# Kernel optimization log

Measured on AMD Instinct MI355X. Metric: run time of the kernel, lower is better.

Reference implementation:

```python
import jax, jax.numpy as jnp
import numpy as np

NUM_HEADS = 16
NEG = -1e9

def setup_inputs() -> dict:
    key = jax.random.key(0)
    ks = jax.random.split(key, 5)
    B, S, D = 4, 2048, 1024
    scale = 1.0 / np.sqrt(D)
    return {
        "x": jax.random.normal(ks[0], (B, S, D), dtype=jnp.float32),
        "WQ": jax.random.normal(ks[1], (D, D), dtype=jnp.float32) * scale,
        "WK": jax.random.normal(ks[2], (D, D), dtype=jnp.float32) * scale,
        "WV": jax.random.normal(ks[3], (D, D), dtype=jnp.float32) * scale,
        "WO": jax.random.normal(ks[4], (D, D), dtype=jnp.float32) * scale,
    }

def _split_heads(t, h):
    # [..., s, h*d] -> [..., h, s, d]
    *lead, s, hd = t.shape
    return jnp.swapaxes(t.reshape(*lead, s, h, hd // h), -3, -2)

def reference(x, WQ, WK, WV, WO):
    h = NUM_HEADS
    S = x.shape[-2]
    # Linear stores weight [out, in]; y = x @ W^T
    Q = _split_heads(x @ WQ.T, h)  # [b,h,s,dk]
    K = _split_heads(x @ WK.T, h)
    V = _split_heads(x @ WV.T, h)
    dk = Q.shape[-1]
    scores = jnp.einsum('bhqd,bhkd->bhqk', Q, K) / jnp.sqrt(jnp.float32(dk))
    causal = jnp.tril(jnp.ones((S, S), dtype=bool))  # allowed positions
    scores = jnp.where(causal, scores, NEG)
    # explicit stable softmax (matches source)
    m = jnp.max(scores, axis=-1, keepdims=True)
    e = jnp.exp(scores - m)
    attn = e / jnp.sum(e, axis=-1, keepdims=True)
    out = jnp.einsum('bhqk,bhkd->bhqd', attn, V)  # [b,h,s,dv]
    out = jnp.swapaxes(out, -3, -2).reshape(*x.shape[:-1], -1)  # [b,s,h*dv]
    return out @ WO.T
```

## Files before the change

### kernel.cpp

```cpp
#include <hip/hip_runtime.h>
#include <stdint.h>
#include <math.h>

typedef __attribute__((ext_vector_type(8))) short bf16x8;
typedef __attribute__((ext_vector_type(4))) short v4s;
typedef __attribute__((ext_vector_type(4))) float f32x4;
typedef __attribute__((ext_vector_type(4))) unsigned short u16x4;
typedef __attribute__((ext_vector_type(2))) unsigned int u32x2;

#define MFMA16(a,b,c)   __builtin_amdgcn_mfma_f32_16x16x32_bf16((a),(b),(c),0,0,0)
#define MFMA16K(a,b,c)  __builtin_amdgcn_mfma_f32_16x16x16bf16_1k((a),(b),(c),0,0,0)

static __device__ __forceinline__ void gld_lds16(const void* g, void* l) {
  __builtin_amdgcn_global_load_lds(
      (const __attribute__((address_space(1))) unsigned int*)g,
      (__attribute__((address_space(3))) unsigned int*)l,
      16, 0, 0);
}

static __device__ __forceinline__ unsigned short f2bf(float f) {
  unsigned int u = __builtin_bit_cast(unsigned int, f);
  return (unsigned short)((u + 0x8000u) >> 16);
}

__global__ __launch_bounds__(256) void cvt_kernel(const float* __restrict__ in,
                                                  unsigned short* __restrict__ out,
                                                  int n4) {
  int i = blockIdx.x * blockDim.x + threadIdx.x;
  int stride = gridDim.x * blockDim.x;
  for (; i < n4; i += stride) {
    float4 v = ((const float4*)in)[i];
    u16x4 o;
    o.x = f2bf(v.x); o.y = f2bf(v.y); o.z = f2bf(v.z); o.w = f2bf(v.w);
    ((u16x4*)out)[i] = o;
  }
}

__global__ __launch_bounds__(256) void cvt4_kernel(const float* __restrict__ w0,
                                                   const float* __restrict__ w1,
                                                   const float* __restrict__ w2,
                                                   const float* __restrict__ w3,
                                                   unsigned short* __restrict__ out) {
  const float* in = (blockIdx.y == 0) ? w0 : (blockIdx.y == 1) ? w1
                  : (blockIdx.y == 2) ? w2 : w3;
  unsigned short* o = out + (size_t)blockIdx.y * 1048576;
  int i = blockIdx.x * blockDim.x + threadIdx.x;
  int stride = gridDim.x * blockDim.x;
  for (; i < 1048576/4; i += stride) {
    float4 v = ((const float4*)in)[i];
    u16x4 t;
    t.x = f2bf(v.x); t.y = f2bf(v.y); t.z = f2bf(v.z); t.w = f2bf(v.w);
    ((u16x4*)o)[i] = t;
  }
}

template<int MODE, typename CT>
__device__ __forceinline__ void gemm_bt_tile(const unsigned short* __restrict__ A,
                                             const unsigned short* __restrict__ Bt,
                                             CT* __restrict__ C,
                                             int m0, int n0)
{
  __shared__ __align__(16) unsigned short As[128*32];
  __shared__ __align__(16) unsigned short Bs[128*32];
  const int tid  = threadIdx.x;
  const int w    = tid >> 6, lane = tid & 63;
  const int quad = lane >> 4, c0 = lane & 15;
  const int wm   = w >> 1, wn = w & 1;

  const unsigned short* ga[2];
  const unsigned short* gb[2];
  int ldsoff[2];
  #pragma unroll
  for (int i = 0; i < 2; ++i) {
    int f = i*4096 + w*1024 + lane*16;
    int r = f >> 6;
    int q = (f >> 4) & 3;
    ga[i] = A  + (m0 + r)*1024 + q*8;
    gb[i] = Bt + (n0 + r)*1024 + q*8;
    ldsoff[i] = i*4096 + w*1024;
  }

  int aAddr[4], bAddr[4];
  #pragma unroll
  for (int t = 0; t < 4; ++t) {
    aAddr[t] = (wm*64 + t*16 + c0)*64 + quad*16;
    bAddr[t] = (wn*64 + t*16 + c0)*64 + quad*16;
  }

  f32x4 acc[4][4];
  #pragma unroll
  for (int i = 0; i < 4; ++i)
    #pragma unroll
    for (int j = 0; j < 4; ++j)
      acc[i][j] = (f32x4){0.f, 0.f, 0.f, 0.f};

  for (int kt = 0; kt < 32; ++kt) {
    __syncthreads();
    #pragma unroll
    for (int i = 0; i < 2; ++i) {
      gld_lds16(ga[i] + kt*32, (char*)As + ldsoff[i]);
      gld_lds16(gb[i] + kt*32, (char*)Bs + ldsoff[i]);
    }
    __syncthreads();

    bf16x8 af[4], bfr[4];
    #pragma unroll
    for (int t = 0; t < 4; ++t) af[t]  = *(const bf16x8*)((const char*)As + aAddr[t]);
    #pragma unroll
    for (int t = 0; t < 4; ++t) bfr[t] = *(const bf16x8*)((const char*)Bs + bAddr[t]);

    #pragma unroll
    for (int mt = 0; mt < 4; ++mt)
      #pragma unroll
      for (int nt = 0; nt < 4; ++nt)
        acc[mt][nt] = MFMA16(af[mt], bfr[nt], acc[mt][nt]);
  }

  const float scl = (MODE == 3) ? 0.1803368801f : 1.0f;
  #pragma unroll
  for (int mt = 0; mt < 4; ++mt) {
    #pragma unroll
    for (int nt = 0; nt < 4; ++nt) {
      if (MODE == 2) {
        u16x4 pk;
        #pragma unroll
        for (int r = 0; r < 4; ++r) pk[r] = f2bf(acc[mt][nt][r]);
        int s0 = m0 + wm*64 + mt*16 + quad*4;
        int gc = n0 + wn*64 + nt*16 + c0;
        int b = s0 >> 11, ss = s0 & 2047;
        int h = gc >> 6, d = gc & 63;
        *(u16x4*)((unsigned short*)C + (size_t)(((b << 4) + h)*64 + d)*2048 + ss) = pk;
      } else {
        #pragma unroll
        for (int r = 0; r < 4; ++r) {
          int gr = m0 + wm*64 + mt*16 + quad*4 + r;
          int gc = n0 + wn*64 + nt*16 + c0;
          if (MODE == 0 || MODE == 3) {
            int b = gr >> 11, s = gr & 2047;
            int h = gc >> 6, d = gc & 63;
            ((unsigned short*)C)[(((b << 4) + h)*2048 + s)*64 + d] = f2bf(acc[mt][nt][r] * scl);
          } else {
            ((float*)C)[gr*1024 + gc] = acc[mt][nt][r];
          }
        }
      }
    }
  }
}

__global__ __launch_bounds__(256) void qkv_kernel(
    const unsigned short* __restrict__ X,
    const unsigned short* __restrict__ WQ, const unsigned short* __restrict__ WK,
    const unsigned short* __restrict__ WV,
    unsigned short* __restrict__ Q, unsigned short* __restrict__ K,
    unsigned short* __restrict__ V)
{
  if (blockIdx.z == 2) {
    gemm_bt_tile<2>(X, WV, V, blockIdx.x*128, blockIdx.y*128);
  } else if (blockIdx.z == 0) {
    gemm_bt_tile<3>(X, WQ, Q, blockIdx.x*128, blockIdx.y*128);
  } else {
    gemm_bt_tile<0>(X, WK, K, blockIdx.x*128, blockIdx.y*128);
  }
}

__global__ __launch_bounds__(256) void proj_kernel(
    const unsigned short* __restrict__ A,
    const unsigned short* __restrict__ WO,
    float* __restrict__ C)
{
  gemm_bt_tile<1>(A, WO, C, blockIdx.x*128, blockIdx.y*128);
}

__global__ __launch_bounds__(256, 2) void attn_kernel(
    const unsigned short* __restrict__ Q,
    const unsigned short* __restrict__ K,
    const unsigned short* __restrict__ Vt,
    unsigned short* __restrict__ O)
{
  __shared__ __align__(16) unsigned short VtL[2][64*128];

  const int tid  = threadIdx.x;
  const int w    = tid >> 6, lane = tid & 63;
  const int quad = lane >> 4, c0 = lane & 15;
  const int bx = blockIdx.y, bh = blockIdx.x;

  const unsigned short* Qh = Q  + (size_t)bh*2048*64;
  const unsigned short* Kh = K  + (size_t)bh*2048*64;
  const unsigned short* Vh = Vt + (size_t)bh*64*2048;

  const unsigned short* vga[4];
  int vldsoff[4];
  #pragma unroll
  for (int i = 0; i < 4; ++i) {
    int cid = i*256 + tid;
    int r = cid >> 4, q = cid & 15;
    int gq = q ^ (r & 15);
    vga[i] = Vh + (size_t)r*2048 + gq*8;
    vldsoff[i] = i*4096 + w*1024;
  }

  const int b = bh >> 4, h = bh & 15;
  bf16x8 kreg[8][2];

  #define ATTN_MK_BODY(mk, Vb, DIAG)                                              \
  {                                                                               \
    f32x4 s0 = (f32x4){0.f,0.f,0.f,0.f}, s1 = (f32x4){0.f,0.f,0.f,0.f};           \
    _Pragma("unroll")                                                             \
    for (int ks = 0; ks < 2; ++ks) {                                              \
      s0 = MFMA16(kreg[mk][ks], qf[0][ks], s0);                                   \
      s1 = MFMA16(kreg[mk][ks], qf[1][ks], s1);                                   \
    }                                                                             \
    if (DIAG) {                                                                   \
      _Pragma("unroll")                                                           \
      for (int r = 0; r < 4; ++r) {                                               \
        int kk = (mk)*16 + quad*4 + r;                                            \
        if (kk > w*32 + c0)      s0[r] = -1e30f;                                  \
        if (kk > w*32 + 16 + c0) s1[r] = -1e30f;                                  \
      }                                                                           \
    }                                                                             \
    float p00 = __builtin_amdgcn_exp2f(s0[0]), p01 = __builtin_amdgcn_exp2f(s0[1]); \
    float p02 = __builtin_amdgcn_exp2f(s0[2]), p03 = __builtin_amdgcn_exp2f(s0[3]); \
    float p10 = __builtin_amdgcn_exp2f(s1[0]), p11 = __builtin_amdgcn_exp2f(s1[1]); \
    float p12 = __builtin_amdgcn_exp2f(s1[2]), p13 = __builtin_amdgcn_exp2f(s1[3]); \
    l_r[0] += (p00 + p01) + (p02 + p03);                                          \
    l_r[1] += (p10 + p11) + (p12 + p13);                                          \
    u32x2 a0, a1;                                                                 \
    a0.x = __builtin_amdgcn_perm(__builtin_bit_cast(unsigned int, p01),           \
                                 __builtin_bit_cast(unsigned int, p00), 0x07060302u); \
    a0.y = __builtin_amdgcn_perm(__builtin_bit_cast(unsigned int, p03),           \
                                 __builtin_bit_cast(unsigned int, p02), 0x07060302u); \
    a1.x = __builtin_amdgcn_perm(__builtin_bit_cast(unsigned int, p11),           \
                                 __builtin_bit_cast(unsigned int, p10), 0x07060302u); \
    a1.y = __builtin_amdgcn_perm(__builtin_bit_cast(unsigned int, p13),           \
                                 __builtin_bit_cast(unsigned int, p12), 0x07060302u); \
    v4s pa0 = __builtin_bit_cast(v4s, a0);                                        \
    v4s pa1 = __builtin_bit_cast(v4s, a1);                                        \
    _Pragma("unroll")                                                             \
    for (int dt = 0; dt < 4; ++dt) {                                              \
      int vr = dt*16 + c0;                                                        \
      int p  = 2*(mk) + (quad >> 1);                                              \
      v4s vb = *(const v4s*)((const char*)(Vb) + vr*256 + ((p ^ c0) * 16) + (quad & 1)*8); \
      o_[0][dt] = MFMA16K(pa0, vb, o_[0][dt]);                                    \
      o_[1][dt] = MFMA16K(pa1, vb, o_[1][dt]);                                    \
    }                                                                             \
  }

  for (int pi = 0; pi < 2; ++pi) {
    const int qt = pi ? bx : 15 - bx;

    bf16x8 qf[2][2];
    #pragma unroll
    for (int mq = 0; mq < 2; ++mq)
      #pragma unroll
      for (int ks = 0; ks < 2; ++ks)
        qf[mq][ks] = *(const bf16x8*)(Qh + (qt*128 + w*32 + mq*16 + c0)*64 + ks*32 + quad*8);

    f32x4 o_[2][4];
    float l_r[2] = {0.f, 0.f};
    #pragma unroll
    for (int mq = 0; mq < 2; ++mq)
      #pragma unroll
      for (int dt = 0; dt < 4; ++dt) o_[mq][dt] = (f32x4){0.f, 0.f, 0.f, 0.f};

    __syncthreads();
    #pragma unroll
    for (int i = 0; i < 4; ++i)
      gld_lds16(vga[i], (char*)VtL[0] + vldsoff[i]);
    #pragma unroll
    for (int mk = 0; mk < 8; ++mk)
      #pragma unroll
      for (int ks = 0; ks < 2; ++ks)
        kreg[mk][ks] = *(const bf16x8*)(Kh + (mk*16 + c0)*64 + ks*32 + quad*8);

    for (int kt = 0; kt < qt; ++kt) {
      __syncthreads();
      #pragma unroll
      for (int i = 0; i < 4; ++i)
        gld_lds16(vga[i] + (kt+1)*128, (char*)VtL[(kt+1)&1] + vldsoff[i]);
      const unsigned short* Vb = VtL[kt & 1];
      #pragma unroll
      for (int mk = 0; mk < 8; ++mk)
        ATTN_MK_BODY(mk, Vb, false)
      #pragma unroll
      for (int mk = 0; mk < 8; ++mk)
        #pragma unroll
        for (int ks = 0; ks < 2; ++ks)
          kreg[mk][ks] = *(const bf16x8*)(Kh + ((kt+1)*128 + mk*16 + c0)*64 + ks*32 + quad*8);
    }

    {
      __syncthreads();
      const unsigned short* Vb = VtL[qt & 1];
      #pragma unroll
      for (int mk = 0; mk < 8; ++mk)
        if (mk < 2*w + 2)
          ATTN_MK_BODY(mk, Vb, true)
    }

    #pragma unroll
    for (int mq = 0; mq < 2; ++mq) {
      l_r[mq] += __shfl_xor(l_r[mq], 16);
      l_r[mq] += __shfl_xor(l_r[mq], 32);
    }
    #pragma unroll
    for (int mt = 0; mt < 2; ++mt) {
      #pragma unroll
      for (int r = 0; r < 4; ++r) {
        float l = __shfl(l_r[mt], quad*4 + r);
        float inv = 1.0f / l;
        int srow = qt*128 + w*32 + mt*16 + quad*4 + r;
        #pragma unroll
        for (int dt = 0; dt < 4; ++dt) {
          int col = h*64 + dt*16 + c0;
          O[((size_t)b*2048 + srow)*1024 + col] = f2bf(o_[mt][dt][r] * inv);
        }
      }
    }
  }
  #undef ATTN_MK_BODY
}

extern "C" void kernel_launch(void* const* d_in, const int* in_sizes, int n_in,
                              void* d_out, int out_size, void* d_ws, size_t ws_size,
                              hipStream_t stream) {
  const float* xf  = (const float*)d_in[0];
  const float* wqf = (const float*)d_in[1];
  const float* wkf = (const float*)d_in[2];
  const float* wvf = (const float*)d_in[3];
  const float* wof = (const float*)d_in[4];
  float* out = (float*)d_out;
  unsigned short* ws = (unsigned short*)d_ws;

  const bool fused = ws_size >= (size_t)58720256;

  if (fused) {
    unsigned short* xb  = ws;
    unsigned short* wb  = ws + 8388608;
    unsigned short* Kw  = ws + 12582912;
    unsigned short* Vw  = ws + 20971520;
    unsigned short* Ow  = xb;
    unsigned short* Qd  = (unsigned short*)out;

    cvt_kernel <<<2048, 256, 0, stream>>>(xf, xb, 8388608/4);
    cvt4_kernel<<<dim3(256, 4), 256, 0, stream>>>(wqf, wkf, wvf, wof, wb);

    qkv_kernel <<<dim3(64, 8, 3), 256, 0, stream>>>(xb, wb, wb + 1048576, wb + 2097152,
                                                    Qd, Kw, Vw);
    attn_kernel<<<dim3(64, 8),    256, 0, stream>>>(Qd, Kw, Vw, Ow);
    proj_kernel<<<dim3(64, 8),    256, 0, stream>>>(Ow, wb + 3145728, out);
  } else {
    unsigned short* xb  = ws;
    unsigned short* wb  = ws + 8388608;
    unsigned short* Kw  = ws + 12582912;
    unsigned short* Vw  = ws + 14680064;
    unsigned short* Ow  = ws + 16777216;

    cvt_kernel <<<2048, 256, 0, stream>>>(xf, xb, 8388608/4);
    cvt4_kernel<<<dim3(256, 4), 256, 0, stream>>>(wqf, wkf, wvf, wof, wb);

    for (int b = 0; b < 4; ++b) {
      const unsigned short* xbb = xb  + (size_t)b * 2048 * 1024;
      float*               outb = out + (size_t)b * 2048 * 1024;
      unsigned short*        Qd = (unsigned short*)outb;
      qkv_kernel <<<dim3(16, 8, 3), 256, 0, stream>>>(xbb, wb, wb + 1048576, wb + 2097152,
                                                      Qd, Kw, Vw);
      attn_kernel<<<dim3(16, 8),    256, 0, stream>>>(Qd, Kw, Vw, Ow);
      proj_kernel<<<dim3(16, 8),    256, 0, stream>>>(Ow, wb + 3145728, outb);
    }
  }
}
```

Baseline: 262.1 us.

## Stage K tiles through swizzled double-buffered LDS instead of per-wave register loads

K tiles were loaded straight from global memory into registers by every wave. They are now copied asynchronously into a double-buffered LDS buffer with an XOR swizzle, alongside the existing V staging, and read from LDS right before each MFMA. This removes the redundant per-wave global K loads and the large kreg register array. It also raises the priority of the compute section with s_setprio. In exchange, LDS use doubles to 64KB per block, which could limit occupancy at 2 blocks per CU, and every MFMA step now adds LDS reads.

```diff
diff --git a/kernel.cpp b/kernel.cpp
--- a/kernel.cpp
+++ b/kernel.cpp
@@ -179,6 +179,7 @@
     unsigned short* __restrict__ O)
 {
   __shared__ __align__(16) unsigned short VtL[2][64*128];
+  __shared__ __align__(16) unsigned short KL[2][128*64];
 
   const int tid  = threadIdx.x;
   const int w    = tid >> 6, lane = tid & 63;
@@ -190,27 +191,31 @@
   const unsigned short* Vh = Vt + (size_t)bh*64*2048;
 
   const unsigned short* vga[4];
-  int vldsoff[4];
+  const unsigned short* kga[4];
+  int ldso[4];
   #pragma unroll
   for (int i = 0; i < 4; ++i) {
     int cid = i*256 + tid;
-    int r = cid >> 4, q = cid & 15;
-    int gq = q ^ (r & 15);
-    vga[i] = Vh + (size_t)r*2048 + gq*8;
-    vldsoff[i] = i*4096 + w*1024;
+    int vr = cid >> 4, vq = cid & 15;
+    vga[i] = Vh + (size_t)vr*2048 + (vq ^ (vr & 15))*8;
+    int kr = cid >> 3, kq = cid & 7;
+    kga[i] = Kh + (size_t)kr*64 + (kq ^ (kr & 7))*8;
+    ldso[i] = i*4096 + w*1024;
   }
 
   const int b = bh >> 4, h = bh & 15;
-  bf16x8 kreg[8][2];
-
-  #define ATTN_MK_BODY(mk, Vb, DIAG)                                              \
+
+  #define ATTN_MK_BODY(mk, Kb, Vb, DIAG)                                          \
   {                                                                               \
+    bf16x8 ka0 = *(const bf16x8*)((const char*)(Kb) + ((mk)*16 + c0)*128          \
+                                  + (((0*4 + quad) ^ (c0 & 7)) * 16));            \
+    bf16x8 ka1 = *(const bf16x8*)((const char*)(Kb) + ((mk)*16 + c0)*128          \
+                                  + (((1*4 + quad) ^ (c0 & 7)) * 16));            \
     f32x4 s0 = (f32x4){0.f,0.f,0.f,0.f}, s1 = (f32x4){0.f,0.f,0.f,0.f};           \
-    _Pragma("unroll")                                                             \
-    for (int ks = 0; ks < 2; ++ks) {                                              \
-      s0 = MFMA16(kreg[mk][ks], qf[0][ks], s0);                                   \
-      s1 = MFMA16(kreg[mk][ks], qf[1][ks], s1);                                   \
-    }                                                                             \
+    s0 = MFMA16(ka0, qf[0][0], s0);                                               \
+    s1 = MFMA16(ka0, qf[1][0], s1);                                               \
+    s0 = MFMA16(ka1, qf[0][1], s0);                                               \
+    s1 = MFMA16(ka1, qf[1][1], s1);                                               \
     if (DIAG) {                                                                   \
       _Pragma("unroll")                                                           \
       for (int r = 0; r < 4; ++r) {                                               \
@@ -265,37 +270,37 @@
 
     __syncthreads();
     #pragma unroll
-    for (int i = 0; i < 4; ++i)
-      gld_lds16(vga[i], (char*)VtL[0] + vldsoff[i]);
-    #pragma unroll
-    for (int mk = 0; mk < 8; ++mk)
-      #pragma unroll
-      for (int ks = 0; ks < 2; ++ks)
-        kreg[mk][ks] = *(const bf16x8*)(Kh + (mk*16 + c0)*64 + ks*32 + quad*8);
+    for (int i = 0; i < 4; ++i) {
+      gld_lds16(vga[i], (char*)VtL[0] + ldso[i]);
+      gld_lds16(kga[i], (char*)KL[0]  + ldso[i]);
+    }
 
     for (int kt = 0; kt < qt; ++kt) {
       __syncthreads();
       #pragma unroll
-      for (int i = 0; i < 4; ++i)
-        gld_lds16(vga[i] + (kt+1)*128, (char*)VtL[(kt+1)&1] + vldsoff[i]);
+      for (int i = 0; i < 4; ++i) {
+        gld_lds16(vga[i] + (kt+1)*128,  (char*)VtL[(kt+1)&1] + ldso[i]);
+        gld_lds16(kga[i] + (kt+1)*8192, (char*)KL[(kt+1)&1]  + ldso[i]);
+      }
       const unsigned short* Vb = VtL[kt & 1];
+      const unsigned short* Kb = KL[kt & 1];
+      __builtin_amdgcn_s_setprio(1);
       #pragma unroll
       for (int mk = 0; mk < 8; ++mk)
-        ATTN_MK_BODY(mk, Vb, false)
-      #pragma unroll
-      for (int mk = 0; mk < 8; ++mk)
-        #pragma unroll
-        for (int ks = 0; ks < 2; ++ks)
-          kreg[mk][ks] = *(const bf16x8*)(Kh + ((kt+1)*128 + mk*16 + c0)*64 + ks*32 + quad*8);
+        ATTN_MK_BODY(mk, Kb, Vb, false)
+      __builtin_amdgcn_s_setprio(0);
     }
 
     {
       __syncthreads();
       const unsigned short* Vb = VtL[qt & 1];
+      const unsigned short* Kb = KL[qt & 1];
+      __builtin_amdgcn_s_setprio(1);
       #pragma unroll
       for (int mk = 0; mk < 8; ++mk)
         if (mk < 2*w + 2)
-          ATTN_MK_BODY(mk, Vb, true)
+          ATTN_MK_BODY(mk, Kb, Vb, true)
+      __builtin_amdgcn_s_setprio(0);
     }
 
     #pragma unroll
```

After: 237.8 us. 1.1x faster.
